# Optimization experiments

Hardware: AMD Instinct MI355X
Metric: run time of the kernel (lower is better)

The kernel has to match this reference:

```python
import jax, jax.numpy as jnp
import numpy as np

BATCH = 256
SEQ = 2048        # sequences (in_features of each per-channel Linear)
C = 32            # input_size (number of independent channels/layers)
EMB = 2048        # embedding_dim (out_features)


def setup_inputs() -> dict:
    key = jax.random.key(0)
    kx, kw, kb = jax.random.split(key, 3)
    x = jax.random.normal(kx, (BATCH, SEQ, C), dtype=jnp.float32)
    # PyTorch nn.Linear init: U(-1/sqrt(fan_in), 1/sqrt(fan_in))
    bound = 1.0 / np.sqrt(SEQ)
    W = jax.random.uniform(kw, (C, SEQ, EMB), minval=-bound, maxval=bound, dtype=jnp.float32)
    b = jax.random.uniform(kb, (C, EMB), minval=-bound, maxval=bound, dtype=jnp.float32)
    return {"x": x, "W": W, "b": b}


def reference(x, W, b):
    # x: (B, S, C) -> transpose to (B, C, S); per-channel Linear + ReLU.
    # Grouped GEMM: out[b,c,e] = relu(sum_s x[b,s,c] * W[c,s,e] + b[c,e])
    xc = jnp.transpose(x, (0, 2, 1))                 # (B, C, S)
    out = jnp.einsum('bcs,cse->bce', xc, W) + b      # (B, C, E)
    return jax.nn.relu(out)
```

## Files before the change

### kernel.cpp

```cpp
#include <hip/hip_runtime.h>

#define BATCH 256
#define SEQ   2048
#define NC    32
#define EMB   2048
#define NT    32

typedef unsigned short ushort_t;
using f32x4  = __attribute__((ext_vector_type(4))) float;
using bf16x8 = __attribute__((ext_vector_type(8))) short;

using u32_gl = __attribute__((address_space(1))) const unsigned int;
using u32_ld = __attribute__((address_space(3))) unsigned int;

__device__ __forceinline__ unsigned int f2bf(float f) {
  unsigned int u = __float_as_uint(f);
  u += 0x7FFFu + ((u >> 16) & 1u);
  return u >> 16;
}

__global__ __launch_bounds__(256) void transpose_x_kernel(
    const float* __restrict__ x, ushort_t* __restrict__ xT) {
  __shared__ float tile[64][33];
  const int b  = blockIdx.x >> 5;
  const int st = blockIdx.x & 31;
  const int t  = threadIdx.x;
  const float* src = x + ((size_t)b * SEQ + (size_t)st * 64) * NC;
#pragma unroll
  for (int i = 0; i < 2; ++i) {
    int idx = t + i * 256;
    float4 v = reinterpret_cast<const float4*>(src)[idx];
    int s = idx >> 3;
    int c = (idx & 7) * 4;
    tile[s][c + 0] = v.x; tile[s][c + 1] = v.y;
    tile[s][c + 2] = v.z; tile[s][c + 3] = v.w;
  }
  __syncthreads();
  const int c  = t >> 3;
  const int si = (t & 7) * 8;
  unsigned int q[4];
#pragma unroll
  for (int p = 0; p < 4; ++p) {
    unsigned int h0 = f2bf(tile[si + 2 * p + 0][c]);
    unsigned int h1 = f2bf(tile[si + 2 * p + 1][c]);
    q[p] = h0 | (h1 << 16);
  }
  ushort_t* dst = xT + (size_t)c * (BATCH * SEQ) + (size_t)b * SEQ + st * 64 + si;
  *reinterpret_cast<uint4*>(dst) = make_uint4(q[0], q[1], q[2], q[3]);
}

template <int P>
__device__ __forceinline__ void gemm_iter(
    int t, const ushort_t* __restrict__ xTc, const float* __restrict__ Wc,
    char* AldsB, char* BldsB, f32x4 (&wv)[2][4], f32x4 (&acc)[4][4],
    int tid, int wr, int g, int lm, int e0) {
  const int srow4 = tid >> 4;
  const int e4    = tid & 15;

  {
    const int tn = (t + 1) & (NT - 1);
    const float* wp = Wc + (size_t)(tn * 64 + srow4 * 4) * EMB + e0 + e4 * 4;
#pragma unroll
    for (int r = 0; r < 4; ++r)
      wv[P ^ 1][r] = *reinterpret_cast<const f32x4*>(wp + (size_t)r * EMB);
  }

  asm volatile("s_waitcnt vmcnt(12)" ::: "memory");
#pragma unroll
  for (int i = 0; i < 4; ++i) {
    const int e_local = e4 * 4 + i;
    unsigned int q0 = f2bf(wv[P][0][i]) | (f2bf(wv[P][1][i]) << 16);
    unsigned int q1 = f2bf(wv[P][2][i]) | (f2bf(wv[P][3][i]) << 16);
    int byte = (e_local * 128 + srow4 * 8) ^ ((e_local & 7) << 4);
    *reinterpret_cast<uint2*>(BldsB + P * 8192 + byte) = make_uint2(q0, q1);
  }

  asm volatile("s_waitcnt lgkmcnt(0)" ::: "memory");
  __builtin_amdgcn_s_barrier();

  {
    const int s0n = ((t + 1) & (NT - 1)) * 64;
#pragma unroll
    for (int i = 0; i < 8; ++i) {
      int ch   = i * 256 + tid;
      int m    = ch >> 3;
      int slot = (ch & 7) ^ (m & 7);
      const ushort_t* src = xTc + (size_t)m * SEQ + s0n + slot * 8;
      __builtin_amdgcn_global_load_lds(
          (u32_gl*)src, (u32_ld*)(AldsB + (P ^ 1) * 32768 + ch * 16), 16, 0, 0);
    }
  }

  asm volatile("s_waitcnt vmcnt(12)" ::: "memory");
  __builtin_amdgcn_sched_barrier(0);

  __builtin_amdgcn_s_barrier();

#pragma unroll
  for (int ks = 0; ks < 2; ++ks) {
    bf16x8 af[4], bfr[4];
#pragma unroll
    for (int mi = 0; mi < 4; ++mi) {
      int m_local = wr * 64 + mi * 16 + lm;
      int byte = (m_local * 128 + (ks * 4 + g) * 16) ^ ((m_local & 7) << 4);
      af[mi] = *reinterpret_cast<const bf16x8*>(AldsB + P * 32768 + byte);
    }
#pragma unroll
    for (int ni = 0; ni < 4; ++ni) {
      int e_local = ni * 16 + lm;
      int byte = (e_local * 128 + (ks * 4 + g) * 16) ^ ((e_local & 7) << 4);
      bfr[ni] = *reinterpret_cast<const bf16x8*>(BldsB + P * 8192 + byte);
    }
#pragma unroll
    for (int mi = 0; mi < 4; ++mi)
#pragma unroll
      for (int ni = 0; ni < 4; ++ni)
        acc[mi][ni] = __builtin_amdgcn_mfma_f32_16x16x32_bf16(
            af[mi], bfr[ni], acc[mi][ni], 0, 0, 0);
  }
}

__global__ __launch_bounds__(256, 2) void grouped_gemm_pipe(
    const ushort_t* __restrict__ xT,
    const float* __restrict__ W,
    const float* __restrict__ bias,
    float* __restrict__ out) {
  __shared__ ushort_t Alds[2][256 * 64];
  __shared__ ushort_t Blds[2][64 * 64];

  const int bid = (blockIdx.x & 7) * 128 + (blockIdx.x >> 3);
  const int c   = bid >> 5;
  const int et  = bid & 31;
  const int e0  = et * 64;

  const int tid  = threadIdx.x;
  const int wr   = tid >> 6;
  const int lane = tid & 63;
  const int g    = lane >> 4;
  const int lm   = lane & 15;

  const float* Wc = W + (size_t)c * SEQ * EMB;
  const ushort_t* xTc = xT + (size_t)c * (BATCH * SEQ);
  char* AldsB = (char*)&Alds[0][0];
  char* BldsB = (char*)&Blds[0][0];

  f32x4 wv[2][4];
  f32x4 acc[4][4];
#pragma unroll
  for (int i = 0; i < 4; ++i)
#pragma unroll
    for (int j = 0; j < 4; ++j) acc[i][j] = (f32x4){0.f, 0.f, 0.f, 0.f};

  {
    const int srow4 = tid >> 4;
    const int e4    = tid & 15;
    const float* wp = Wc + (size_t)(srow4 * 4) * EMB + e0 + e4 * 4;
#pragma unroll
    for (int r = 0; r < 4; ++r)
      wv[0][r] = *reinterpret_cast<const f32x4*>(wp + (size_t)r * EMB);
#pragma unroll
    for (int i = 0; i < 8; ++i) {
      int ch   = i * 256 + tid;
      int m    = ch >> 3;
      int slot = (ch & 7) ^ (m & 7);
      const ushort_t* src = xTc + (size_t)m * SEQ + slot * 8;
      __builtin_amdgcn_global_load_lds(
          (u32_gl*)src, (u32_ld*)(AldsB + ch * 16), 16, 0, 0);
    }
  }

  for (int t = 0; t < NT; t += 2) {
    gemm_iter<0>(t,     xTc, Wc, AldsB, BldsB, wv, acc, tid, wr, g, lm, e0);
    gemm_iter<1>(t + 1, xTc, Wc, AldsB, BldsB, wv, acc, tid, wr, g, lm, e0);
  }

  asm volatile("s_waitcnt vmcnt(0)" ::: "memory");

  const float* bc = bias + (size_t)c * EMB;
#pragma unroll
  for (int ni = 0; ni < 4; ++ni) {
    const int e = e0 + ni * 16 + lm;
    const float bv = bc[e];
#pragma unroll
    for (int mi = 0; mi < 4; ++mi) {
      f32x4 a = acc[mi][ni];
      const int mbase = wr * 64 + mi * 16 + g * 4;
#pragma unroll
      for (int r = 0; r < 4; ++r) {
        float v = a[r] + bv;
        v = fmaxf(v, 0.f);
        out[((size_t)(mbase + r) * NC + c) * EMB + e] = v;
      }
    }
  }
}

__global__ __launch_bounds__(256, 2) void grouped_gemm_fallback(
    const float* __restrict__ x, const float* __restrict__ W,
    const float* __restrict__ bias, float* __restrict__ out) {
  __shared__ ushort_t Alds[128 * 64];
  __shared__ ushort_t Blds[128 * 64];
  const int bid = blockIdx.x;
  const int c   = bid >> 5;
  const int et  = (bid >> 1) & 15;
  const int bt  = bid & 1;
  const int b0  = bt * 128;
  const int e0  = et * 128;
  const int tid  = threadIdx.x;
  const int w    = tid >> 6;
  const int wr   = w >> 1;
  const int wc   = w & 1;
  const int lane = tid & 63;
  const int g    = lane >> 4;
  const int lm   = lane & 15;
  const float* Wc = W + (size_t)c * SEQ * EMB;
  const int srow8 = tid >> 5;
  const int e4    = tid & 31;
  f32x4 acc[4][4];
#pragma unroll
  for (int i = 0; i < 4; ++i)
#pragma unroll
    for (int j = 0; j < 4; ++j) acc[i][j] = (f32x4){0.f, 0.f, 0.f, 0.f};
  for (int s0 = 0; s0 < SEQ; s0 += 64) {
#pragma unroll
    for (int i = 0; i < 4; ++i) {
      int ch   = i * 256 + tid;
      int m    = ch >> 3;
      int slot = (ch & 7) ^ (m & 7);
      const float* src = x + (size_t)(b0 + m) * (SEQ * NC)
                           + (size_t)(s0 + slot * 8) * NC + c;
      unsigned int q[4];
#pragma unroll
      for (int p = 0; p < 4; ++p) {
        unsigned int h0 = f2bf(src[(2 * p + 0) * NC]);
        unsigned int h1 = f2bf(src[(2 * p + 1) * NC]);
        q[p] = h0 | (h1 << 16);
      }
      *reinterpret_cast<uint4*>((char*)&Alds[0] + ch * 16) =
          make_uint4(q[0], q[1], q[2], q[3]);
    }
    {
      const float* wp = Wc + (size_t)(s0 + srow8 * 8) * EMB + e0 + e4 * 4;
      f32x4 wvv[8];
#pragma unroll
      for (int r = 0; r < 8; ++r)
        wvv[r] = *reinterpret_cast<const f32x4*>(wp + (size_t)r * EMB);
#pragma unroll
      for (int i = 0; i < 4; ++i) {
        const int e_local = e4 * 4 + i;
        unsigned int q0 = f2bf(wvv[0][i]) | (f2bf(wvv[1][i]) << 16);
        unsigned int q1 = f2bf(wvv[2][i]) | (f2bf(wvv[3][i]) << 16);
        unsigned int q2 = f2bf(wvv[4][i]) | (f2bf(wvv[5][i]) << 16);
        unsigned int q3 = f2bf(wvv[6][i]) | (f2bf(wvv[7][i]) << 16);
        int byte = (e_local * 128 + srow8 * 16) ^ ((e_local & 7) << 4);
        *reinterpret_cast<uint4*>((char*)&Blds[0] + byte) =
            make_uint4(q0, q1, q2, q3);
      }
    }
    __syncthreads();
#pragma unroll
    for (int ks = 0; ks < 2; ++ks) {
      bf16x8 af[4], bfr[4];
#pragma unroll
      for (int mi = 0; mi < 4; ++mi) {
        int m_local = wr * 64 + mi * 16 + lm;
        int byte = (m_local * 128 + (ks * 4 + g) * 16) ^ ((m_local & 7) << 4);
        af[mi] = *reinterpret_cast<const bf16x8*>((const char*)&Alds[0] + byte);
      }
#pragma unroll
      for (int ni = 0; ni < 4; ++ni) {
        int e_local = wc * 64 + ni * 16 + lm;
        int byte = (e_local * 128 + (ks * 4 + g) * 16) ^ ((e_local & 7) << 4);
        bfr[ni] = *reinterpret_cast<const bf16x8*>((const char*)&Blds[0] + byte);
      }
#pragma unroll
      for (int mi = 0; mi < 4; ++mi)
#pragma unroll
        for (int ni = 0; ni < 4; ++ni)
          acc[mi][ni] = __builtin_amdgcn_mfma_f32_16x16x32_bf16(
              af[mi], bfr[ni], acc[mi][ni], 0, 0, 0);
    }
    __syncthreads();
  }
  const float* bc = bias + (size_t)c * EMB;
#pragma unroll
  for (int ni = 0; ni < 4; ++ni) {
    const int e = e0 + wc * 64 + ni * 16 + lm;
    const float bv = bc[e];
#pragma unroll
    for (int mi = 0; mi < 4; ++mi) {
      f32x4 a = acc[mi][ni];
      const int mbase = b0 + wr * 64 + mi * 16 + g * 4;
#pragma unroll
      for (int r = 0; r < 4; ++r) {
        float v = a[r] + bv;
        v = fmaxf(v, 0.f);
        out[((size_t)(mbase + r) * NC + c) * EMB + e] = v;
      }
    }
  }
}

extern "C" void kernel_launch(void* const* d_in, const int* in_sizes, int n_in,
                              void* d_out, int out_size, void* d_ws, size_t ws_size,
                              hipStream_t stream) {
  const float* x    = (const float*)d_in[0];
  const float* W    = (const float*)d_in[1];
  const float* bias = (const float*)d_in[2];
  float* out        = (float*)d_out;

  const size_t xT_bytes = (size_t)NC * BATCH * SEQ * sizeof(ushort_t);

  if (ws_size >= xT_bytes) {
    ushort_t* xT = (ushort_t*)d_ws;
    transpose_x_kernel<<<BATCH * (SEQ / 64), 256, 0, stream>>>(x, xT);
    grouped_gemm_pipe<<<NC * (EMB / 64), 256, 0, stream>>>(xT, W, bias, out);
  } else {
    grouped_gemm_fallback<<<NC * 2 * (EMB / 128), 256, 0, stream>>>(x, W, bias, out);
  }
}
```

Baseline: 174.4 us.

## Enlarge GEMM block tile to 256x256 with 512 threads and 4x2 wave grid

```diff
diff --git a/kernel.cpp b/kernel.cpp
--- a/kernel.cpp
+++ b/kernel.cpp
@@ -18,6 +18,8 @@
   u += 0x7FFFu + ((u >> 16) & 1u);
   return u >> 16;
 }
+
+#define SB() __builtin_amdgcn_sched_barrier(0)
 
 __global__ __launch_bounds__(256) void transpose_x_kernel(
     const float* __restrict__ x, ushort_t* __restrict__ xT) {
@@ -52,134 +54,138 @@
 template <int P>
 __device__ __forceinline__ void gemm_iter(
     int t, const ushort_t* __restrict__ xTc, const float* __restrict__ Wc,
-    char* AldsB, char* BldsB, f32x4 (&wv)[2][4], f32x4 (&acc)[4][4],
-    int tid, int wr, int g, int lm, int e0) {
-  const int srow4 = tid >> 4;
-  const int e4    = tid & 15;
+    char* Alds, char* Blds, f32x4 (&wv)[2][8], f32x4 (&acc)[4][8],
+    int tid, int wr, int wc, int g, int lm, int e0) {
+  const int w    = tid >> 6;
+  const int lane = tid & 63;
 
   {
     const int tn = (t + 1) & (NT - 1);
-    const float* wp = Wc + (size_t)(tn * 64 + srow4 * 4) * EMB + e0 + e4 * 4;
-#pragma unroll
-    for (int r = 0; r < 4; ++r)
+    const float* wp = Wc + (size_t)(tn * 64 + w * 8) * EMB + e0 + lane * 4;
+#pragma unroll
+    for (int r = 0; r < 8; ++r)
       wv[P ^ 1][r] = *reinterpret_cast<const f32x4*>(wp + (size_t)r * EMB);
   }
+  SB();
 
   asm volatile("s_waitcnt vmcnt(12)" ::: "memory");
+  SB();
+
 #pragma unroll
   for (int i = 0; i < 4; ++i) {
-    const int e_local = e4 * 4 + i;
+    const int e = lane * 4 + i;
     unsigned int q0 = f2bf(wv[P][0][i]) | (f2bf(wv[P][1][i]) << 16);
     unsigned int q1 = f2bf(wv[P][2][i]) | (f2bf(wv[P][3][i]) << 16);
-    int byte = (e_local * 128 + srow4 * 8) ^ ((e_local & 7) << 4);
-    *reinterpret_cast<uint2*>(BldsB + P * 8192 + byte) = make_uint2(q0, q1);
-  }
-
+    unsigned int q2 = f2bf(wv[P][4][i]) | (f2bf(wv[P][5][i]) << 16);
+    unsigned int q3 = f2bf(wv[P][6][i]) | (f2bf(wv[P][7][i]) << 16);
+    int byte = e * 128 + ((w ^ (lane & 7)) << 4);
+    *reinterpret_cast<uint4*>(Blds + P * 32768 + byte) = make_uint4(q0, q1, q2, q3);
+  }
   asm volatile("s_waitcnt lgkmcnt(0)" ::: "memory");
   __builtin_amdgcn_s_barrier();
 
   {
     const int s0n = ((t + 1) & (NT - 1)) * 64;
 #pragma unroll
-    for (int i = 0; i < 8; ++i) {
-      int ch   = i * 256 + tid;
+    for (int i = 0; i < 4; ++i) {
+      int ch   = i * 512 + tid;
       int m    = ch >> 3;
       int slot = (ch & 7) ^ (m & 7);
       const ushort_t* src = xTc + (size_t)m * SEQ + s0n + slot * 8;
       __builtin_amdgcn_global_load_lds(
-          (u32_gl*)src, (u32_ld*)(AldsB + (P ^ 1) * 32768 + ch * 16), 16, 0, 0);
+          (u32_gl*)src, (u32_ld*)(Alds + (P ^ 1) * 32768 + ch * 16), 16, 0, 0);
     }
   }
 
   asm volatile("s_waitcnt vmcnt(12)" ::: "memory");
-  __builtin_amdgcn_sched_barrier(0);
+  SB();
 
   __builtin_amdgcn_s_barrier();
 
 #pragma unroll
   for (int ks = 0; ks < 2; ++ks) {
-    bf16x8 af[4], bfr[4];
+    bf16x8 af[4];
 #pragma unroll
     for (int mi = 0; mi < 4; ++mi) {
       int m_local = wr * 64 + mi * 16 + lm;
       int byte = (m_local * 128 + (ks * 4 + g) * 16) ^ ((m_local & 7) << 4);
-      af[mi] = *reinterpret_cast<const bf16x8*>(AldsB + P * 32768 + byte);
-    }
-#pragma unroll
-    for (int ni = 0; ni < 4; ++ni) {
-      int e_local = ni * 16 + lm;
-      int byte = (e_local * 128 + (ks * 4 + g) * 16) ^ ((e_local & 7) << 4);
-      bfr[ni] = *reinterpret_cast<const bf16x8*>(BldsB + P * 8192 + byte);
-    }
-#pragma unroll
-    for (int mi = 0; mi < 4; ++mi)
-#pragma unroll
-      for (int ni = 0; ni < 4; ++ni)
+      af[mi] = *reinterpret_cast<const bf16x8*>(Alds + P * 32768 + byte);
+    }
+#pragma unroll
+    for (int ni = 0; ni < 8; ++ni) {
+      int e_local = wc * 128 + ni * 16 + lm;
+      int byte = e_local * 128 + (((ks * 4 + g) ^ ((e_local >> 2) & 7)) << 4);
+      bf16x8 bfr = *reinterpret_cast<const bf16x8*>(Blds + P * 32768 + byte);
+#pragma unroll
+      for (int mi = 0; mi < 4; ++mi)
         acc[mi][ni] = __builtin_amdgcn_mfma_f32_16x16x32_bf16(
-            af[mi], bfr[ni], acc[mi][ni], 0, 0, 0);
-  }
-}
-
-__global__ __launch_bounds__(256, 2) void grouped_gemm_pipe(
+            af[mi], bfr, acc[mi][ni], 0, 0, 0);
+    }
+  }
+}
+
+__global__ __launch_bounds__(512, 1) void grouped_gemm_pipe(
     const ushort_t* __restrict__ xT,
     const float* __restrict__ W,
     const float* __restrict__ bias,
     float* __restrict__ out) {
-  __shared__ ushort_t Alds[2][256 * 64];
-  __shared__ ushort_t Blds[2][64 * 64];
-
-  const int bid = (blockIdx.x & 7) * 128 + (blockIdx.x >> 3);
-  const int c   = bid >> 5;
-  const int et  = bid & 31;
-  const int e0  = et * 64;
+  __shared__ ushort_t AldsU[2][256 * 64];
+  __shared__ ushort_t BldsU[2][256 * 64];
+
+  const int bid = (blockIdx.x & 7) * 32 + (blockIdx.x >> 3);
+  const int c   = bid >> 3;
+  const int et  = bid & 7;
+  const int e0  = et * 256;
 
   const int tid  = threadIdx.x;
-  const int wr   = tid >> 6;
+  const int w    = tid >> 6;
+  const int wr   = w >> 1;
+  const int wc   = w & 1;
   const int lane = tid & 63;
   const int g    = lane >> 4;
   const int lm   = lane & 15;
 
   const float* Wc = W + (size_t)c * SEQ * EMB;
   const ushort_t* xTc = xT + (size_t)c * (BATCH * SEQ);
-  char* AldsB = (char*)&Alds[0][0];
-  char* BldsB = (char*)&Blds[0][0];
-
-  f32x4 wv[2][4];
-  f32x4 acc[4][4];
+  char* Alds = (char*)&AldsU[0][0];
+  char* Blds = (char*)&BldsU[0][0];
+
+  f32x4 wv[2][8];
+  f32x4 acc[4][8];
 #pragma unroll
   for (int i = 0; i < 4; ++i)
 #pragma unroll
-    for (int j = 0; j < 4; ++j) acc[i][j] = (f32x4){0.f, 0.f, 0.f, 0.f};
+    for (int j = 0; j < 8; ++j) acc[i][j] = (f32x4){0.f, 0.f, 0.f, 0.f};
 
   {
-    const int srow4 = tid >> 4;
-    const int e4    = tid & 15;
-    const float* wp = Wc + (size_t)(srow4 * 4) * EMB + e0 + e4 * 4;
-#pragma unroll
-    for (int r = 0; r < 4; ++r)
+    const float* wp = Wc + (size_t)(w * 8) * EMB + e0 + lane * 4;
+#pragma unroll
+    for (int r = 0; r < 8; ++r)
       wv[0][r] = *reinterpret_cast<const f32x4*>(wp + (size_t)r * EMB);
-#pragma unroll
-    for (int i = 0; i < 8; ++i) {
-      int ch   = i * 256 + tid;
+    SB();
+#pragma unroll
+    for (int i = 0; i < 4; ++i) {
+      int ch   = i * 512 + tid;
       int m    = ch >> 3;
       int slot = (ch & 7) ^ (m & 7);
       const ushort_t* src = xTc + (size_t)m * SEQ + slot * 8;
       __builtin_amdgcn_global_load_lds(
-          (u32_gl*)src, (u32_ld*)(AldsB + ch * 16), 16, 0, 0);
-    }
+          (u32_gl*)src, (u32_ld*)(Alds + ch * 16), 16, 0, 0);
+    }
+    SB();
   }
 
   for (int t = 0; t < NT; t += 2) {
-    gemm_iter<0>(t,     xTc, Wc, AldsB, BldsB, wv, acc, tid, wr, g, lm, e0);
-    gemm_iter<1>(t + 1, xTc, Wc, AldsB, BldsB, wv, acc, tid, wr, g, lm, e0);
+    gemm_iter<0>(t,     xTc, Wc, Alds, Blds, wv, acc, tid, wr, wc, g, lm, e0);
+    gemm_iter<1>(t + 1, xTc, Wc, Alds, Blds, wv, acc, tid, wr, wc, g, lm, e0);
   }
 
   asm volatile("s_waitcnt vmcnt(0)" ::: "memory");
 
   const float* bc = bias + (size_t)c * EMB;
 #pragma unroll
-  for (int ni = 0; ni < 4; ++ni) {
-    const int e = e0 + ni * 16 + lm;
+  for (int ni = 0; ni < 8; ++ni) {
+    const int e = e0 + wc * 128 + ni * 16 + lm;
     const float bv = bc[e];
 #pragma unroll
     for (int mi = 0; mi < 4; ++mi) {
@@ -314,7 +320,7 @@
   if (ws_size >= xT_bytes) {
     ushort_t* xT = (ushort_t*)d_ws;
     transpose_x_kernel<<<BATCH * (SEQ / 64), 256, 0, stream>>>(x, xT);
-    grouped_gemm_pipe<<<NC * (EMB / 64), 256, 0, stream>>>(xT, W, bias, out);
+    grouped_gemm_pipe<<<NC * (EMB / 256), 512, 0, stream>>>(xT, W, bias, out);
   } else {
     grouped_gemm_fallback<<<NC * 2 * (EMB / 128), 256, 0, stream>>>(x, W, bias, out);
   }
```

Result: slower. 230.6 us (+32.2%).
